# Kernel tuning notes

Measured on AMD Instinct MI355X. Metric: run time of the kernel, lower is better.

The kernel has to match this reference:

```python
import jax, jax.numpy as jnp
import numpy as np
from jax import lax

B = 512
THRESHOLD = 0.5
CFG = [64, 64, 'M', 128, 128, 'M', 256, 256, 256, 'M', 512, 512, 512, 'M', 512, 512, 512, 'M']  # VGG16


def _conv_relu(x, w, b):
    # x: [B,C,H,W], w: [O,I,3,3] (torch OIHW layout), pad=1 stride=1
    y = lax.conv_general_dilated(x, w, (1, 1), 'SAME',
                                 dimension_numbers=('NCHW', 'OIHW', 'NCHW'))
    return jax.nn.relu(y + b[None, :, None, None])


def _maxpool2(x):
    return lax.reduce_window(x, -jnp.inf, lax.max, (1, 1, 2, 2), (1, 1, 2, 2), 'VALID')


def _features(x, ws, bs):
    i = 0
    for c in CFG:
        if c == 'M':
            x = _maxpool2(x)
        else:
            x = _conv_relu(x, ws[i], bs[i])
            i += 1
    return x  # [B,512,1,1]


def _gcn(distance):
    # Faithful translation, including the source bug: 'onetensor' is zeros_like,
    # so mask==0 everywhere and A_hat collapses to the identity.
    n = distance.shape[0]
    zero = jnp.zeros_like(distance)
    one = jnp.zeros_like(distance)  # bug in original: torch.zeros_like for onetensor
    adj = jnp.where(distance > THRESHOLD, distance, zero)
    mask = jnp.where(distance > THRESHOLD, one, zero)
    idx = lax.top_k(adj, 10)[1]                                   # [n,10]
    top10 = jnp.zeros_like(adj).at[jnp.arange(n)[:, None], idx].set(1.0)
    top10 = top10 * mask
    a_hat = top10 + jnp.eye(n, dtype=distance.dtype)
    d_inv = jnp.diag(1.0 / jnp.sum(a_hat, axis=1))
    return lax.stop_gradient(a_hat @ d_inv)                        # [n,n]


def _forward(x, target, conv_ws, conv_bs, lin1_w, lin1_b, lin2_w, lin2_b, cls_w, cls_b):
    feat = _features(x, conv_ws, conv_bs).reshape(x.shape[0], -1)  # [B,512]
    h = jax.nn.relu(feat @ lin1_w + lin1_b)                        # [B,256]
    low = h @ lin2_w + lin2_b                                      # [B,128]
    graph_pre = jax.nn.sigmoid(low @ low.T)                        # [B,B]
    graph_gt = (target[:, None] == target[None, :]).astype(jnp.float32)
    mat = _gcn(graph_pre)                                          # [B,B], detached
    out = (mat @ feat) @ cls_w + cls_b                             # [B,10]
    return out, graph_pre, graph_gt


def setup_inputs() -> dict:
    key = jax.random.key(0)
    ks = iter(jax.random.split(key, 64))
    inp = {}
    inp['x'] = jax.random.normal(next(ks), (B, 3, 32, 32), dtype=jnp.float32)
    inp['target'] = jax.random.randint(next(ks), (B,), 0, 10)
    in_c, i = 3, 0
    for c in CFG:
        if c == 'M':
            continue
        scale = 1.0 / np.sqrt(in_c * 9.0)
        inp['conv%d_w' % i] = jax.random.normal(next(ks), (c, in_c, 3, 3), dtype=jnp.float32) * scale
        inp['conv%d_b' % i] = jnp.zeros((c,), dtype=jnp.float32)
        in_c, i = c, i + 1
    inp['lin1_w'] = jax.random.normal(next(ks), (512, 256), dtype=jnp.float32) * (1.0 / np.sqrt(512.0))
    inp['lin1_b'] = jnp.zeros((256,), dtype=jnp.float32)
    inp['lin2_w'] = jax.random.normal(next(ks), (256, 128), dtype=jnp.float32) * (1.0 / np.sqrt(256.0))
    inp['lin2_b'] = jnp.zeros((128,), dtype=jnp.float32)
    inp['cls_w'] = jax.random.normal(next(ks), (512, 10), dtype=jnp.float32) * (1.0 / np.sqrt(512.0))
    inp['cls_b'] = jnp.zeros((10,), dtype=jnp.float32)
    return inp


def reference(x, target,
              conv0_w, conv0_b, conv1_w, conv1_b, conv2_w, conv2_b, conv3_w, conv3_b,
              conv4_w, conv4_b, conv5_w, conv5_b, conv6_w, conv6_b, conv7_w, conv7_b,
              conv8_w, conv8_b, conv9_w, conv9_b, conv10_w, conv10_b, conv11_w, conv11_b,
              conv12_w, conv12_b,
              lin1_w, lin1_b, lin2_w, lin2_b, cls_w, cls_b):
    ws = [conv0_w, conv1_w, conv2_w, conv3_w, conv4_w, conv5_w, conv6_w,
          conv7_w, conv8_w, conv9_w, conv10_w, conv11_w, conv12_w]
    bs = [conv0_b, conv1_b, conv2_b, conv3_b, conv4_b, conv5_b, conv6_b,
          conv7_b, conv8_b, conv9_b, conv10_b, conv11_b, conv12_b]
    return _forward(x, target, ws, bs, lin1_w, lin1_b, lin2_w, lin2_b, cls_w, cls_b)
```

## Files before the change

### kernel.cpp

```cpp
#include <hip/hip_runtime.h>

typedef unsigned short u16;
typedef __bf16 bf16x8 __attribute__((ext_vector_type(8)));
typedef float floatx4 __attribute__((ext_vector_type(4)));

__device__ inline u16 f2bf(float f) {
    return __builtin_bit_cast(u16, (__bf16)f);
}
__device__ inline float bf2f(u16 h) {
    return __uint_as_float(((unsigned int)h) << 16);
}

__device__ __forceinline__ void async_copy16(u16* lds, const u16* g) {
    __builtin_amdgcn_global_load_lds(
        (const __attribute__((address_space(1))) unsigned int*)(uintptr_t)g,
        (__attribute__((address_space(3))) unsigned int*)(unsigned int)(uintptr_t)lds,
        16, 0, 0);
}

__global__ void zero_halo(u16* __restrict__ buf, int Hp, int C, int total8)
{
    int i = blockIdx.x * 256 + threadIdx.x;
    if (i >= total8) return;
    int c8 = i % (C / 8);
    int p  = i / (C / 8);
    int ring = 4 * Hp - 4;
    int h = p % ring;
    int b = p / ring;
    int y, x;
    if (h < Hp)              { y = 0;              x = h; }
    else if (h < 2 * Hp)     { y = Hp - 1;         x = h - Hp; }
    else if (h < 3 * Hp - 2) { y = h - 2 * Hp + 1; x = 0; }
    else                     { y = h - 3 * Hp + 3; x = Hp - 1; }
    uint4 z = make_uint4(0u, 0u, 0u, 0u);
    *(uint4*)(buf + ((size_t)((b * Hp + y) * Hp + x) * C) + c8 * 8) = z;
}

__global__ __launch_bounds__(256) void conv0_kernel(
    const float* __restrict__ x, const float* __restrict__ w,
    const float* __restrict__ bias, u16* __restrict__ out)
{
    __shared__ __align__(16) float xs[3][6][36];
    const int t  = threadIdx.x;
    const int b  = blockIdx.x >> 3;
    const int y0 = (blockIdx.x & 7) * 4;

    for (int i = t; i < 3 * 6 * 36; i += 256) {
        int ci  = i / 216;
        int rem = i % 216;
        int r   = rem / 36;
        int c   = rem % 36;
        int gy  = y0 - 1 + r;
        int gx  = c - 1;
        float v = 0.f;
        if ((unsigned)gy < 32u && (unsigned)gx < 32u)
            v = x[((b * 3 + ci) * 32 + gy) * 32 + gx];
        xs[ci][r][c] = v;
    }
    const int lane = t & 63;
    const int wv   = t >> 6;
    float wr[27];
    #pragma unroll
    for (int k = 0; k < 27; k++) wr[k] = w[lane * 27 + k];
    const float bz = bias[lane];
    __syncthreads();

    const int y = y0 + wv;
    u16* orow = out + ((size_t)((b * 34 + y + 1) * 34 + 1) * 64) + lane;
    for (int xg = 0; xg < 32; xg += 4) {
        float a0 = bz, a1 = bz, a2 = bz, a3 = bz;
        #pragma unroll
        for (int ci = 0; ci < 3; ci++) {
            #pragma unroll
            for (int rr = 0; rr < 3; rr++) {
                const float* row = &xs[ci][wv + rr][0];
                float4 c03 = *(const float4*)(row + xg);
                float2 c45 = *(const float2*)(row + xg + 4);
                float w0 = wr[ci * 9 + rr * 3 + 0];
                float w1 = wr[ci * 9 + rr * 3 + 1];
                float w2 = wr[ci * 9 + rr * 3 + 2];
                a0 += c03.x * w0 + c03.y * w1 + c03.z * w2;
                a1 += c03.y * w0 + c03.z * w1 + c03.w * w2;
                a2 += c03.z * w0 + c03.w * w1 + c45.x * w2;
                a3 += c03.w * w0 + c45.x * w1 + c45.y * w2;
            }
        }
        orow[(xg + 0) * 64] = f2bf(fmaxf(a0, 0.f));
        orow[(xg + 1) * 64] = f2bf(fmaxf(a1, 0.f));
        orow[(xg + 2) * 64] = f2bf(fmaxf(a2, 0.f));
        orow[(xg + 3) * 64] = f2bf(fmaxf(a3, 0.f));
    }
}

struct RepackArgs {
    const float* src[14];
    u16* dst[14];
    int p1[14];
    int p2[14];
    int startBlk[15];
    int nseg;
};

__global__ __launch_bounds__(256) void repack_all(RepackArgs a)
{
    __shared__ __align__(16) u16 lds[9216];
    int blk = blockIdx.x;
    int s = 0;
    #pragma unroll 1
    while (s + 1 < a.nseg && blk >= a.startBlk[s + 1]) s++;
    const int cb = blk - a.startBlk[s];
    const int t  = threadIdx.x;

    if (a.p2[s] == 0) {
        const int Cin = a.p1[s];
        const int logCin = __builtin_ctz(Cin);
        const float* src = a.src[s] + (size_t)cb * 9216;
        u16* dst = a.dst[s] + (size_t)cb * 9216;
        #pragma unroll
        for (int it = 0; it < 9; it++) {
            int j4 = it * 256 + t;
            float4 v = *(const float4*)(src + j4 * 4);
            ushort4 h;
            h.x = f2bf(v.x); h.y = f2bf(v.y); h.z = f2bf(v.z); h.w = f2bf(v.w);
            *(ushort4*)(lds + j4 * 4) = h;
        }
        __syncthreads();
        #pragma unroll
        for (int it = 0; it < 9; it++) {
            int o4   = (it * 256 + t) * 4;
            int ci   = o4 & (Cin - 1);
            int rest = o4 >> logCin;
            int co   = rest / 9;
            int sh   = rest - co * 9;
            int sb   = (co << logCin) * 9 + ci * 9 + sh;
            ushort4 h;
            h.x = lds[sb]; h.y = lds[sb + 9]; h.z = lds[sb + 18]; h.w = lds[sb + 27];
            *(ushort4*)(dst + o4) = h;
        }
    } else {
        const int K = a.p1[s], N = a.p2[s];
        const int ntx = N >> 6;
        const int k0 = (cb / ntx) * 64, n0 = (cb % ntx) * 64;
        const float* src = a.src[s];
        u16* dst = a.dst[s];
        const int r = t >> 4, c4 = (t & 15) * 4;
        #pragma unroll
        for (int rr = 0; rr < 64; rr += 16) {
            float4 v = *(const float4*)(src + (size_t)(k0 + r + rr) * N + n0 + c4);
            u16* p = lds + (r + rr) * 72 + c4;
            p[0] = f2bf(v.x); p[1] = f2bf(v.y); p[2] = f2bf(v.z); p[3] = f2bf(v.w);
        }
        __syncthreads();
        #pragma unroll
        for (int it = 0; it < 2; it++) {
            int ov = it * 256 + t;
            int n  = ov >> 3;
            int kq = (ov & 7) * 8;
            __align__(16) u16 h[8];
            #pragma unroll
            for (int j = 0; j < 8; j++) h[j] = lds[(kq + j) * 72 + n];
            *(uint4*)(dst + (size_t)(n0 + n) * K + k0 + kq) = *(uint4*)h;
        }
    }
}

template <int BM, int BN>
__global__ __launch_bounds__(256) void conv_gemm(
    const u16* __restrict__ in, const u16* __restrict__ wt,
    const float* __restrict__ bias, u16* __restrict__ out,
    float* __restrict__ partial, size_t pstride,
    int H, int Cin, int Cout, int logHW, int logW, int splitN,
    int outPad, int poolMode)
{
    constexpr int BK = 64;
    constexpr int WC = (BM == 256) ? BN : (BN / 2);
    constexpr int NT = WC / 16;
    constexpr int NB_A = BM / 32;
    constexpr int NB_B = BN / 32;
    constexpr int ASZ = BM * BK;
    constexpr int BSZ = BN * BK;
    __shared__ u16 As[2 * ASZ];
    __shared__ u16 Bs[2 * BSZ];

    const int Nblocks = Cout / BN;
    const int per = gridDim.x >> 3;
    const int bid = (blockIdx.x & 7) * per + (blockIdx.x >> 3);
    const int sp   = bid % splitN;
    const int tile = bid / splitN;
    const int m0 = (tile / Nblocks) * BM;
    const int n0 = (tile % Nblocks) * BN;

    const int t    = threadIdx.x;
    const int lane = t & 63;
    const int wave = t >> 6;
    const int quad = lane >> 4;
    const int l16  = lane & 15;
    const int wm   = (BM == 256) ? wave : (wave >> 1);
    const int wn   = (BM == 256) ? 0 : (wave & 1);
    const int W    = H;
    const int Wp   = H + 2;
    const int HW   = 1 << logHW;
    const int col8 = t & 7;
    const int r0   = t >> 3;
    const int scol = col8 ^ (r0 & 7);

    const int CinB = Cin * 2;

    int vA[NB_A];
    #pragma unroll
    for (int j = 0; j < NB_A; j++) {
        int m  = m0 + r0 + 32 * j;
        int b  = m >> logHW;
        int rm = m & (HW - 1);
        int y  = rm >> logW;
        int xx = rm & (W - 1);
        vA[j] = ((b * Wp + y + 1) * Wp + xx + 1) * CinB + scol * 16;
    }
    int vB[NB_B];
    #pragma unroll
    for (int j = 0; j < NB_B; j++)
        vB[j] = (n0 + r0 + 32 * j) * 9 * CinB + scol * 16;

    const int logKB = (Cin == 64) ? 0 : (Cin == 128) ? 1 : (Cin == 256) ? 2 : 3;
    const int KB  = 1 << logKB;
    const int T   = 9 * KB;
    const int len = T / splitN;
    const int it0 = sp * len;

    int s0 = it0 >> logKB;
    int c3 = s0 - (s0 / 3) * 3;
    int ta = ((s0 / 3 - 1) * Wp + (c3 - 1)) * CinB;
    int kb = (it0 & (KB - 1)) * 128;
    int tb = it0 * 128;

    const char* const inB = (const char*)in;
    const char* const wtB = (const char*)wt;

    floatx4 acc[4][NT];
    #pragma unroll
    for (int i = 0; i < 4; i++)
        #pragma unroll
        for (int j = 0; j < NT; j++)
            acc[i][j] = (floatx4){0.f, 0.f, 0.f, 0.f};

    const int sw = (l16 & 7) * 8;

    auto stage = [&](int ua, int tbv, int buf) {
        u16* la = As + buf * ASZ + t * 8;
        u16* lb = Bs + buf * BSZ + t * 8;
        #pragma unroll
        for (int j = 0; j < NB_A; j++)
            async_copy16(la + j * 2048, (const u16*)(inB + (ua + vA[j])));
        #pragma unroll
        for (int j = 0; j < NB_B; j++)
            async_copy16(lb + j * 2048, (const u16*)(wtB + (tbv + vB[j])));
    };
    auto advance = [&]() {
        tb += 128;
        kb += 128;
        if (kb == CinB) {
            kb = 0;
            ta += (c3 == 2) ? (Wp - 2) * CinB : CinB;
            c3 = (c3 == 2) ? 0 : c3 + 1;
        }
    };

    stage(ta + kb, tb, 0);
    advance();
    __syncthreads();

    int cur = 0;
    for (int it = 0; it < len; it++) {
        if (it + 1 < len) {
            stage(ta + kb, tb, cur ^ 1);
            advance();
        }
        const u16* Ab = As + cur * ASZ;
        const u16* Bb = Bs + cur * BSZ;
        #pragma unroll
        for (int kk = 0; kk < BK; kk += 32) {
            bf16x8 af[4], bfv[NT];
            int cbo = kk + quad * 8;
            #pragma unroll
            for (int mt = 0; mt < 4; mt++)
                af[mt] = *(const bf16x8*)(Ab + (wm * 64 + mt * 16 + l16) * 64 + (cbo ^ sw));
            #pragma unroll
            for (int nt = 0; nt < NT; nt++)
                bfv[nt] = *(const bf16x8*)(Bb + (wn * WC + nt * 16 + l16) * 64 + (cbo ^ sw));
            #pragma unroll
            for (int mt = 0; mt < 4; mt++)
                #pragma unroll
                for (int nt = 0; nt < NT; nt++)
                    acc[mt][nt] = __builtin_amdgcn_mfma_f32_16x16x32_bf16(
                        af[mt], bfv[nt], acc[mt][nt], 0, 0, 0);
        }
        __syncthreads();
        cur ^= 1;
    }

    const int ngb = n0 + wn * WC + l16;

    if (splitN > 1) {
        float* pout = partial + (size_t)sp * pstride;
        #pragma unroll
        for (int mt = 0; mt < 4; mt++)
            #pragma unroll
            for (int r = 0; r < 4; r++) {
                int mg = m0 + wm * 64 + mt * 16 + quad * 4 + r;
                float* op = pout + (size_t)mg * Cout + ngb;
                #pragma unroll
                for (int nt = 0; nt < NT; nt++)
                    op[nt * 16] = acc[mt][nt][r];
            }
        return;
    }

    float bzv[NT];
    #pragma unroll
    for (int nt = 0; nt < NT; nt++) bzv[nt] = bias[ngb + nt * 16];

    if (poolMode) {
        const int Hpo = (H >> 1) + 2;
        if (logW == 5) {
            #pragma unroll
            for (int mt = 0; mt < 2; mt++)
                #pragma unroll
                for (int rp = 0; rp < 2; rp++) {
                    int m1 = m0 + wm * 64 + mt * 16 + quad * 4 + 2 * rp;
                    int b  = m1 >> logHW;
                    int rm = m1 & (HW - 1);
                    int yp = (rm >> logW) >> 1;
                    int xp = (rm & (W - 1)) >> 1;
                    u16* op = out + (size_t)((b * Hpo + yp + 1) * Hpo + xp + 1) * Cout + ngb;
                    #pragma unroll
                    for (int nt = 0; nt < NT; nt++) {
                        float v = fmaxf(
                            fmaxf(acc[mt][nt][2 * rp], acc[mt][nt][2 * rp + 1]),
                            fmaxf(acc[mt + 2][nt][2 * rp], acc[mt + 2][nt][2 * rp + 1]));
                        op[nt * 16] = f2bf(fmaxf(v + bzv[nt], 0.f));
                    }
                }
        } else if (logW == 4) {
            #pragma unroll
            for (int mtp = 0; mtp < 2; mtp++)
                #pragma unroll
                for (int rp = 0; rp < 2; rp++) {
                    int mt = 2 * mtp;
                    int m1 = m0 + wm * 64 + mt * 16 + quad * 4 + 2 * rp;
                    int b  = m1 >> logHW;
                    int rm = m1 & (HW - 1);
                    int yp = (rm >> logW) >> 1;
                    int xp = (rm & (W - 1)) >> 1;
                    u16* op = out + (size_t)((b * Hpo + yp + 1) * Hpo + xp + 1) * Cout + ngb;
                    #pragma unroll
                    for (int nt = 0; nt < NT; nt++) {
                        float v = fmaxf(
                            fmaxf(acc[mt][nt][2 * rp], acc[mt][nt][2 * rp + 1]),
                            fmaxf(acc[mt + 1][nt][2 * rp], acc[mt + 1][nt][2 * rp + 1]));
                        op[nt * 16] = f2bf(fmaxf(v + bzv[nt], 0.f));
                    }
                }
        } else {
            #pragma unroll
            for (int mt = 0; mt < 4; mt++)
                #pragma unroll
                for (int rp = 0; rp < 2; rp++) {
                    int m1 = m0 + wm * 64 + mt * 16 + quad * 4 + 2 * rp;
                    int b  = m1 >> logHW;
                    int rm = m1 & (HW - 1);
                    int yp = (rm >> logW) >> 1;
                    int xp = (rm & (W - 1)) >> 1;
                    u16* op = out + (size_t)((b * Hpo + yp + 1) * Hpo + xp + 1) * Cout + ngb;
                    #pragma unroll
                    for (int nt = 0; nt < NT; nt++) {
                        float a = fmaxf(acc[mt][nt][2 * rp], acc[mt][nt][2 * rp + 1]);
                        float p = __shfl_xor(a, 32, 64);
                        float v = fmaxf(a, p);
                        if (quad < 2)
                            op[nt * 16] = f2bf(fmaxf(v + bzv[nt], 0.f));
                    }
                }
        }
        return;
    }

    #pragma unroll
    for (int mt = 0; mt < 4; mt++) {
        #pragma unroll
        for (int r = 0; r < 4; r++) {
            int mg = m0 + wm * 64 + mt * 16 + quad * 4 + r;
            size_t obase;
            if (outPad) {
                int b  = mg >> logHW;
                int rm = mg & (HW - 1);
                int y  = rm >> logW;
                int xx = rm & (W - 1);
                obase = (size_t)((b * Wp + y + 1) * Wp + xx + 1) * Cout;
            } else {
                obase = (size_t)mg * Cout;
            }
            u16* op = out + obase + ngb;
            #pragma unroll
            for (int nt = 0; nt < NT; nt++)
                op[nt * 16] = f2bf(fmaxf(acc[mt][nt][r] + bzv[nt], 0.f));
        }
    }
}

template <int BM, int BN, int W, int CIN>
__global__ __launch_bounds__(256) void conv_halo(
    const u16* __restrict__ in, const u16* __restrict__ wt,
    const float* __restrict__ bias, u16* __restrict__ out,
    int outPad, int poolMode)
{
    constexpr int BK = 64;
    constexpr int WC = (BM == 256) ? BN : (BN / 2);
    constexpr int NT = WC / 16;
    constexpr int NB_B = BN / 32;
    constexpr int BSZ = BN * BK;
    constexpr int Wp = W + 2;
    constexpr int R  = BM / W;
    constexpr int P  = (R + 2) * Wp;
    constexpr int CinB = CIN * 2;
    constexpr int CH = CinB / 16;
    constexpr int LOG_CH = (CH == 8) ? 3 : 4;
    constexpr int HALO_CHUNKS = P * CH;
    constexpr int ROUNDS = (HALO_CHUNKS + 255) / 256;
    constexpr int logW = (W == 32) ? 5 : 4;
    constexpr int logHW = 2 * logW;
    constexpr int HW = 1 << logHW;
    constexpr int KB = CIN / 64;
    constexpr int T  = 9 * KB;

    __shared__ __align__(16) u16 Ah[P * CH * 8];
    __shared__ __align__(16) u16 Bs[2 * BSZ];

    constexpr int Nblocks = 1;
    static_assert(true, "");
    const int per = gridDim.x >> 3;
    const int bid = (blockIdx.x & 7) * per + (blockIdx.x >> 3);
    const int m0 = (bid / Nblocks) * BM;
    const int n0 = (bid % Nblocks) * BN;

    const int t    = threadIdx.x;
    const int lane = t & 63;
    const int wave = t >> 6;
    const int quad = lane >> 4;
    const int l16  = lane & 15;
    const int wm   = (BM == 256) ? wave : (wave >> 1);
    const int wn   = (BM == 256) ? 0 : (wave & 1);
    const int col8 = t & 7;
    const int r0   = t >> 3;
    const int scol = col8 ^ (r0 & 7);

    const int b  = m0 >> logHW;
    const int y0 = (m0 & (HW - 1)) >> logW;

    const char* hsrc = (const char*)in + (size_t)((b * Wp + y0) * Wp) * CinB;
    #pragma unroll
    for (int rd = 0; rd < ROUNDS; rd++) {
        int i = rd * 256 + t;
        if ((HALO_CHUNKS % 256 == 0) || i < HALO_CHUNKS) {
            int pp   = i >> LOG_CH;
            int si   = i ^ (pp & 7);
            async_copy16(Ah + i * 8, (const u16*)(hsrc + (size_t)si * 16));
        }
    }

    int vB[NB_B];
    #pragma unroll
    for (int j = 0; j < NB_B; j++)
        vB[j] = (n0 + r0 + 32 * j) * 9 * CinB + scol * 16;
    const char* const wtB = (const char*)wt;
    auto stageB = [&](int tbv, int buf) {
        u16* lb = Bs + buf * BSZ + t * 8;
        #pragma unroll
        for (int j = 0; j < NB_B; j++)
            async_copy16(lb + j * 2048, (const u16*)(wtB + (tbv + vB[j])));
    };

    int pBase[4];
    #pragma unroll
    for (int mt = 0; mt < 4; mt++) {
        int dm = wm * 64 + mt * 16 + l16;
        pBase[mt] = (dm >> logW) * Wp + (dm & (W - 1));
    }

    floatx4 acc[4][NT];
    #pragma unroll
    for (int i = 0; i < 4; i++)
        #pragma unroll
        for (int j = 0; j < NT; j++)
            acc[i][j] = (floatx4){0.f, 0.f, 0.f, 0.f};

    const int sw = (l16 & 7) * 8;
    const char* const AhB = (const char*)Ah;

    stageB(0, 0);
    __syncthreads();

    int cur = 0, tb = 128;
    int pOff = 0, c3 = 0, cb = 0;
    for (int it = 0; it < T; it++) {
        if (it + 1 < T) { stageB(tb, cur ^ 1); tb += 128; }
        const int pO = pOff, cbv = cb;
        cb += 128;
        if (cb == CinB) {
            cb = 0;
            pOff += (c3 == 2) ? (Wp - 2) : 1;
            c3 = (c3 == 2) ? 0 : c3 + 1;
        }

        bf16x8 af[2][4];
        #pragma unroll
        for (int mt = 0; mt < 4; mt++) {
            int p  = pBase[mt] + pO;
            int pc = p & 7;
            int ab = p * CinB + cbv;
            #pragma unroll
            for (int kk2 = 0; kk2 < 2; kk2++) {
                int kq = kk2 * 4 + quad;
                af[kk2][mt] = *(const bf16x8*)(AhB + ab + ((kq ^ pc) << 4));
            }
        }

        const u16* Bb = Bs + cur * BSZ;
        #pragma unroll
        for (int kk2 = 0; kk2 < 2; kk2++) {
            int cbo = kk2 * 32 + quad * 8;
            bf16x8 bfv[NT];
            #pragma unroll
            for (int nt = 0; nt < NT; nt++)
                bfv[nt] = *(const bf16x8*)(Bb + (wn * WC + nt * 16 + l16) * 64 + (cbo ^ sw));
            #pragma unroll
            for (int mt = 0; mt < 4; mt++)
                #pragma unroll
                for (int nt = 0; nt < NT; nt++)
                    acc[mt][nt] = __builtin_amdgcn_mfma_f32_16x16x32_bf16(
                        af[kk2][mt], bfv[nt], acc[mt][nt], 0, 0, 0);
        }
        __syncthreads();
        cur ^= 1;
    }

    const int ngb = n0 + wn * WC + l16;
    float bzv[NT];
    #pragma unroll
    for (int nt = 0; nt < NT; nt++) bzv[nt] = bias[ngb + nt * 16];
    const int Cout = BN;
    const int H = W;

    if (poolMode) {
        const int Hpo = (H >> 1) + 2;
        if (logW == 5) {
            #pragma unroll
            for (int mt = 0; mt < 2; mt++)
                #pragma unroll
                for (int rp = 0; rp < 2; rp++) {
                    int m1 = m0 + wm * 64 + mt * 16 + quad * 4 + 2 * rp;
                    int bb = m1 >> logHW;
                    int rm = m1 & (HW - 1);
                    int yp = (rm >> logW) >> 1;
                    int xp = (rm & (W - 1)) >> 1;
                    u16* op = out + (size_t)((bb * Hpo + yp + 1) * Hpo + xp + 1) * Cout + ngb;
                    #pragma unroll
                    for (int nt = 0; nt < NT; nt++) {
                        float v = fmaxf(
                            fmaxf(acc[mt][nt][2 * rp], acc[mt][nt][2 * rp + 1]),
                            fmaxf(acc[mt + 2][nt][2 * rp], acc[mt + 2][nt][2 * rp + 1]));
                        op[nt * 16] = f2bf(fmaxf(v + bzv[nt], 0.f));
                    }
                }
        } else {
            #pragma unroll
            for (int mtp = 0; mtp < 2; mtp++)
                #pragma unroll
                for (int rp = 0; rp < 2; rp++) {
                    int mt = 2 * mtp;
                    int m1 = m0 + wm * 64 + mt * 16 + quad * 4 + 2 * rp;
                    int bb = m1 >> logHW;
                    int rm = m1 & (HW - 1);
                    int yp = (rm >> logW) >> 1;
                    int xp = (rm & (W - 1)) >> 1;
                    u16* op = out + (size_t)((bb * Hpo + yp + 1) * Hpo + xp + 1) * Cout + ngb;
                    #pragma unroll
                    for (int nt = 0; nt < NT; nt++) {
                        float v = fmaxf(
                            fmaxf(acc[mt][nt][2 * rp], acc[mt][nt][2 * rp + 1]),
                            fmaxf(acc[mt + 1][nt][2 * rp], acc[mt + 1][nt][2 * rp + 1]));
                        op[nt * 16] = f2bf(fmaxf(v + bzv[nt], 0.f));
                    }
                }
        }
        return;
    }

    #pragma unroll
    for (int mt = 0; mt < 4; mt++) {
        #pragma unroll
        for (int r = 0; r < 4; r++) {
            int mg = m0 + wm * 64 + mt * 16 + quad * 4 + r;
            size_t obase;
            if (outPad) {
                int bb = mg >> logHW;
                int rm = mg & (HW - 1);
                int y  = rm >> logW;
                int xx = rm & (W - 1);
                obase = (size_t)((bb * Wp + y + 1) * Wp + xx + 1) * Cout;
            } else {
                obase = (size_t)mg * Cout;
            }
            u16* op = out + obase + ngb;
            #pragma unroll
            for (int nt = 0; nt < NT; nt++)
                op[nt * 16] = f2bf(fmaxf(acc[mt][nt][r] + bzv[nt], 0.f));
        }
    }
}

__global__ void reduce_split(const float* __restrict__ partial,
                             const float* __restrict__ bias, u16* __restrict__ out,
                             int MN, int C, int logC, int splitN, size_t pstride,
                             int H, int logHW, int logW, int outPad)
{
    int i4 = (blockIdx.x * 256 + threadIdx.x) * 4;
    if (i4 >= MN) return;
    float4 s = *(const float4*)(partial + i4);
    for (int sp = 1; sp < splitN; sp++) {
        float4 p = *(const float4*)(partial + (size_t)sp * pstride + i4);
        s.x += p.x; s.y += p.y; s.z += p.z; s.w += p.w;
    }
    int n = i4 & (C - 1);
    int m = i4 >> logC;
    size_t obase;
    if (outPad) {
        int Wp = H + 2;
        int b  = m >> logHW;
        int rm = m & ((1 << logHW) - 1);
        int y  = rm >> logW;
        int xx = rm & (H - 1);
        obase = (size_t)((b * Wp + y + 1) * Wp + xx + 1) * C;
    } else {
        obase = (size_t)m * C;
    }
    ushort4 o;
    o.x = f2bf(fmaxf(s.x + bias[n + 0], 0.f));
    o.y = f2bf(fmaxf(s.y + bias[n + 1], 0.f));
    o.z = f2bf(fmaxf(s.z + bias[n + 2], 0.f));
    o.w = f2bf(fmaxf(s.w + bias[n + 3], 0.f));
    *(ushort4*)(out + obase + n) = o;
}

__global__ void reduce_pool(const float* __restrict__ partial,
                            const float* __restrict__ bias, u16* __restrict__ out,
                            int total4, int C, int splitN, size_t pstride,
                            int H, int outPad)
{
    int idx = blockIdx.x * 256 + threadIdx.x;
    if (idx >= total4) return;
    int c4 = idx % (C / 4);
    int p  = idx / (C / 4);
    int Ho = H >> 1;
    int xp = p % Ho; p /= Ho;
    int yp = p % Ho;
    int b  = p / Ho;
    int n  = c4 * 4;
    float4 best;
    bool first = true;
    #pragma unroll
    for (int dy = 0; dy < 2; dy++)
        #pragma unroll
        for (int dx = 0; dx < 2; dx++) {
            int m = (b * H + 2 * yp + dy) * H + 2 * xp + dx;
            const float* q = partial + (size_t)m * C + n;
            float4 s = *(const float4*)q;
            for (int sp = 1; sp < splitN; sp++) {
                float4 pp = *(const float4*)(q + (size_t)sp * pstride);
                s.x += pp.x; s.y += pp.y; s.z += pp.z; s.w += pp.w;
            }
            if (first) { best = s; first = false; }
            else {
                best.x = fmaxf(best.x, s.x); best.y = fmaxf(best.y, s.y);
                best.z = fmaxf(best.z, s.z); best.w = fmaxf(best.w, s.w);
            }
        }
    size_t obase;
    if (outPad) {
        int Hpo = Ho + 2;
        obase = (size_t)((b * Hpo + yp + 1) * Hpo + xp + 1) * C;
    } else {
        obase = (size_t)((b * Ho + yp) * Ho + xp) * C;
    }
    ushort4 o;
    o.x = f2bf(fmaxf(best.x + bias[n + 0], 0.f));
    o.y = f2bf(fmaxf(best.y + bias[n + 1], 0.f));
    o.z = f2bf(fmaxf(best.z + bias[n + 2], 0.f));
    o.w = f2bf(fmaxf(best.w + bias[n + 3], 0.f));
    *(ushort4*)(out + obase + n) = o;
}

template <bool RELU, bool OUTBF>
__global__ __launch_bounds__(256) void gemm64(
    const u16* __restrict__ A, const u16* __restrict__ Bt,
    const float* __restrict__ bias, void* __restrict__ outv,
    int M, int N, int K)
{
    constexpr int LDP = 72;
    __shared__ u16 As[64 * LDP];
    __shared__ u16 Bs[64 * LDP];

    const int nb = N >> 6;
    const int m0 = (blockIdx.x / nb) * 64;
    const int n0 = (blockIdx.x % nb) * 64;
    const int t = threadIdx.x, lane = t & 63, wave = t >> 6;
    const int quad = lane >> 4, l16 = lane & 15;
    const int wm = wave >> 1, wn = wave & 1;
    const int col8 = t & 7, r0 = t >> 3;

    floatx4 acc[2][2];
    #pragma unroll
    for (int i = 0; i < 2; i++)
        #pragma unroll
        for (int j = 0; j < 2; j++)
            acc[i][j] = (floatx4){0.f, 0.f, 0.f, 0.f};

    for (int kb = 0; kb < K; kb += 64) {
        #pragma unroll
        for (int j = 0; j < 2; j++) {
            int row = r0 + 32 * j;
            *(uint4*)(As + row * LDP + col8 * 8) =
                *(const uint4*)(A + (size_t)(m0 + row) * K + kb + col8 * 8);
            *(uint4*)(Bs + row * LDP + col8 * 8) =
                *(const uint4*)(Bt + (size_t)(n0 + row) * K + kb + col8 * 8);
        }
        __syncthreads();
        #pragma unroll
        for (int kk = 0; kk < 64; kk += 32) {
            bf16x8 af[2], bfv[2];
            #pragma unroll
            for (int mt = 0; mt < 2; mt++)
                af[mt] = *(const bf16x8*)(As + (wm * 32 + mt * 16 + l16) * LDP + kk + quad * 8);
            #pragma unroll
            for (int nt = 0; nt < 2; nt++)
                bfv[nt] = *(const bf16x8*)(Bs + (wn * 32 + nt * 16 + l16) * LDP + kk + quad * 8);
            #pragma unroll
            for (int mt = 0; mt < 2; mt++)
                #pragma unroll
                for (int nt = 0; nt < 2; nt++)
                    acc[mt][nt] = __builtin_amdgcn_mfma_f32_16x16x32_bf16(
                        af[mt], bfv[nt], acc[mt][nt], 0, 0, 0);
        }
        __syncthreads();
    }
    #pragma unroll
    for (int mt = 0; mt < 2; mt++) {
        #pragma unroll
        for (int nt = 0; nt < 2; nt++) {
            #pragma unroll
            for (int r = 0; r < 4; r++) {
                int mg = m0 + wm * 32 + mt * 16 + quad * 4 + r;
                int ng = n0 + wn * 32 + nt * 16 + l16;
                float v = acc[mt][nt][r] + bias[ng];
                if (RELU) v = fmaxf(v, 0.f);
                if (OUTBF) ((u16*)outv)[(size_t)mg * N + ng] = f2bf(v);
                else       ((float*)outv)[(size_t)mg * N + ng] = v;
            }
        }
    }
}

__global__ __launch_bounds__(256) void graph_tile(
    const float* __restrict__ low, const int* __restrict__ target,
    float* __restrict__ gpre, float* __restrict__ ggt)
{
    __shared__ float Al[64 * 132];
    __shared__ float Bl[128 * 68];
    const int t = threadIdx.x;
    const int gr0 = (blockIdx.x >> 3) * 64;
    const int gc0 = (blockIdx.x & 7) * 64;

    #pragma unroll
    for (int j = 0; j < 32; j++) {
        int flat = t + 256 * j;
        int k = flat & 127;
        int rc = flat >> 7;
        Al[rc * 132 + k] = low[(size_t)(gr0 + rc) * 128 + k];
        Bl[k * 68 + rc]  = low[(size_t)(gc0 + rc) * 128 + k];
    }
    __syncthreads();

    const int tx = t & 15, ty = t >> 4;
    float acc[4][4];
    #pragma unroll
    for (int r = 0; r < 4; r++)
        #pragma unroll
        for (int c = 0; c < 4; c++) acc[r][c] = 0.f;

    for (int k = 0; k < 128; k++) {
        float a[4], b[4];
        #pragma unroll
        for (int r = 0; r < 4; r++) a[r] = Al[(ty * 4 + r) * 132 + k];
        #pragma unroll
        for (int c = 0; c < 4; c++) b[c] = Bl[k * 68 + tx * 4 + c];
        #pragma unroll
        for (int r = 0; r < 4; r++)
            #pragma unroll
            for (int c = 0; c < 4; c++) acc[r][c] += a[r] * b[c];
    }
    #pragma unroll
    for (int r = 0; r < 4; r++) {
        int row = gr0 + ty * 4 + r;
        int tr  = target[row];
        float4 gp, gg;
        float* pp = (float*)&gp;
        float* gg_ = (float*)&gg;
        #pragma unroll
        for (int c = 0; c < 4; c++) {
            pp[c]  = 1.f / (1.f + __expf(-acc[r][c]));
            gg_[c] = (tr == target[gc0 + tx * 4 + c]) ? 1.f : 0.f;
        }
        *(float4*)(gpre + (size_t)row * 512 + gc0 + tx * 4) = gp;
        *(float4*)(ggt  + (size_t)row * 512 + gc0 + tx * 4) = gg;
    }
}

__global__ __launch_bounds__(256) void cls_kernel(
    const u16* __restrict__ feat, const float* __restrict__ w,
    const float* __restrict__ bias, float* __restrict__ out)
{
    __shared__ float ws[5120];
    const int t = threadIdx.x;
    for (int i = t; i < 5120; i += 256) ws[i] = w[i];
    __syncthreads();
    const int lane = t & 63;
    const int row  = blockIdx.x * 4 + (t >> 6);
    float a[10];
    #pragma unroll
    for (int j = 0; j < 10; j++) a[j] = 0.f;
    #pragma unroll
    for (int i = 0; i < 8; i++) {
        int k = i * 64 + lane;
        float f = bf2f(feat[(size_t)row * 512 + k]);
        #pragma unroll
        for (int j = 0; j < 10; j++) a[j] += f * ws[k * 10 + j];
    }
    #pragma unroll
    for (int j = 0; j < 10; j++)
        #pragma unroll
        for (int off = 32; off > 0; off >>= 1)
            a[j] += __shfl_down(a[j], off, 64);
    if (lane == 0) {
        #pragma unroll
        for (int j = 0; j < 10; j++) out[row * 10 + j] = a[j] + bias[j];
    }
}

extern "C" void kernel_launch(void* const* d_in, const int* in_sizes, int n_in,
                              void* d_out, int out_size, void* d_ws, size_t ws_size,
                              hipStream_t stream)
{
    const float* x      = (const float*)d_in[0];
    const int*   target = (const int*)d_in[1];
    const float* conv_w[13];
    const float* conv_b[13];
    for (int i = 0; i < 13; i++) {
        conv_w[i] = (const float*)d_in[2 + 2 * i];
        conv_b[i] = (const float*)d_in[3 + 2 * i];
    }
    const float* lin1_w = (const float*)d_in[28];
    const float* lin1_b = (const float*)d_in[29];
    const float* lin2_w = (const float*)d_in[30];
    const float* lin2_b = (const float*)d_in[31];
    const float* cls_w  = (const float*)d_in[32];
    const float* cls_b  = (const float*)d_in[33];
    float* out = (float*)d_out;

    static const int cin_arr[13]  = {3, 64, 64, 128, 128, 256, 256, 256, 512, 512, 512, 512, 512};
    static const int cout_arr[13] = {64, 64, 128, 128, 256, 256, 256, 512, 512, 512, 512, 512, 512};

    char* ws = (char*)d_ws;
    size_t off = 0;
    const size_t R0SZ = (size_t)512 * 34 * 34 * 64 * 2;
    const size_t R1SZ = (size_t)512 * 34 * 34 * 64 * 2;
    char* R0raw = ws + off; off += R0SZ;
    char* R1raw = ws + off; off += R1SZ;
    u16* R0 = (u16*)R0raw;
    u16* R1 = (u16*)R1raw;
    float* PA = (float*)(R0raw + 20971520);
    float* PB = (float*)(R1raw + 20971520);
    u16* wt[13];
    for (int i = 1; i < 13; i++) {
        wt[i] = (u16*)(ws + off);
        off += (size_t)cout_arr[i] * 9 * cin_arr[i] * 2;
    }
    u16* wtl1 = (u16*)(ws + off); off += (size_t)256 * 512 * 2;
    u16* wtl2 = (u16*)(ws + off); off += (size_t)128 * 256 * 2;
    u16* hbuf = (u16*)(ws + off); off += (size_t)512 * 256 * 2;
    float* lowbuf = (float*)(ws + off); off += (size_t)512 * 128 * 4;

    RepackArgs ra;
    int nb = 0, blk = 0;
    ra.startBlk[0] = 0;
    for (int i = 1; i < 13; i++) {
        ra.src[nb] = conv_w[i];
        ra.dst[nb] = wt[i];
        ra.p1[nb] = cin_arr[i];
        ra.p2[nb] = 0;
        blk += cout_arr[i] * cin_arr[i] / 1024;
        nb++; ra.startBlk[nb] = blk;
    }
    ra.src[nb] = lin1_w; ra.dst[nb] = wtl1; ra.p1[nb] = 512; ra.p2[nb] = 256;
    blk += (512 / 64) * (256 / 64);
    nb++; ra.startBlk[nb] = blk;
    ra.src[nb] = lin2_w; ra.dst[nb] = wtl2; ra.p1[nb] = 256; ra.p2[nb] = 128;
    blk += (256 / 64) * (128 / 64);
    nb++; ra.startBlk[nb] = blk;
    ra.nseg = nb;
    repack_all<<<blk, 256, 0, stream>>>(ra);

    auto zh = [&](u16* buf, int Hp, int C) {
        int total8 = 512 * (4 * Hp - 4) * (C / 8);
        zero_halo<<<(total8 + 255) / 256, 256, 0, stream>>>(buf, Hp, C, total8);
    };
    auto launch_conv = [&](int li, int Hl, int bm, int bn, u16* inb, u16* outb,
                           float* part, int splitN, int outPad, int poolMode) {
        int Cin = cin_arr[li], Cout = cout_arr[li];
        int M = 512 * Hl * Hl;
        int logW = __builtin_ctz(Hl);
        int logHW = 2 * logW;
        size_t pstride = (size_t)M * Cout;
        int grid = (M / bm) * (Cout / bn) * splitN;
        if (bm == 256) {
            conv_gemm<256, 64><<<grid, 256, 0, stream>>>(
                inb, wt[li], conv_b[li], outb, part, pstride,
                Hl, Cin, Cout, logHW, logW, splitN, outPad, poolMode);
        } else if (bn == 128) {
            conv_gemm<128, 128><<<grid, 256, 0, stream>>>(
                inb, wt[li], conv_b[li], outb, part, pstride,
                Hl, Cin, Cout, logHW, logW, splitN, outPad, poolMode);
        } else {
            conv_gemm<128, 64><<<grid, 256, 0, stream>>>(
                inb, wt[li], conv_b[li], outb, part, pstride,
                Hl, Cin, Cout, logHW, logW, splitN, outPad, poolMode);
        }
    };
    auto launch_reduce = [&](int li, int Hl, u16* outb, float* part, int splitN, int outPad) {
        int Cout = cout_arr[li];
        int M = 512 * Hl * Hl;
        int logW = __builtin_ctz(Hl);
        size_t pstride = (size_t)M * Cout;
        int MN = M * Cout;
        reduce_split<<<(MN / 4 + 255) / 256, 256, 0, stream>>>(
            part, conv_b[li], outb, MN, Cout, __builtin_ctz(Cout),
            splitN, pstride, Hl, 2 * logW, logW, outPad);
    };
    auto launch_reduce_pool = [&](int li, int Hl, u16* outb, float* part, int splitN, int outPad) {
        int Cout = cout_arr[li];
        int M = 512 * Hl * Hl;
        size_t pstride = (size_t)M * Cout;
        int total4 = 512 * (Hl / 2) * (Hl / 2) * Cout / 4;
        reduce_pool<<<(total4 + 255) / 256, 256, 0, stream>>>(
            part, conv_b[li], outb, total4, Cout, splitN, pstride, Hl, outPad);
    };

    zh(R0, 34, 64);
    conv0_kernel<<<512 * 8, 256, 0, stream>>>(x, conv_w[0], conv_b[0], R0);

    zh(R1, 18, 64);
    conv_halo<256, 64, 32, 64><<<2048, 256, 0, stream>>>(
        R0, wt[1], conv_b[1], R1, 0, 1);
    zh(R0, 18, 128);
    conv_halo<128, 128, 16, 64><<<1024, 256, 0, stream>>>(
        R1, wt[2], conv_b[2], R0, 1, 0);
    zh(R1, 10, 128);
    conv_halo<128, 128, 16, 128><<<1024, 256, 0, stream>>>(
        R0, wt[3], conv_b[3], R1, 0, 1);
    zh(R0, 10, 256);
    launch_conv(4, 8, 128, 128, R1, R0, nullptr, 1, 1, 0);
    zh(R1, 10, 256);
    launch_conv(5, 8, 128, 128, R0, R1, nullptr, 1, 1, 0);
    zh(R0, 6, 256);
    launch_conv(6, 8, 128, 128, R1, R0, nullptr, 1, 0, 1);
    zh(R1, 6, 512);
    launch_conv(7, 4, 128, 128, R0, R1, PB, 2, 1, 0);
    launch_reduce(7, 4, R1, PB, 2, 1);
    zh(R0, 6, 512);
    launch_conv(8, 4, 128, 128, R1, R0, PA, 2, 1, 0);
    launch_reduce(8, 4, R0, PA, 2, 1);
    zh(R1, 4, 512);
    launch_conv(9, 4, 128, 128, R0, R1, PB, 2, 0, 0);
    launch_reduce_pool(9, 4, R1, PB, 2, 1);
    zh(R0, 4, 512);
    launch_conv(10, 2, 128, 64, R1, R0, PA, 4, 1, 0);
    launch_reduce(10, 2, R0, PA, 4, 1);
    zh(R1, 4, 512);
    launch_conv(11, 2, 128, 64, R0, R1, PB, 4, 1, 0);
    launch_reduce(11, 2, R1, PB, 4, 1);
    launch_conv(12, 2, 128, 64, R1, R0, PA, 4, 0, 0);
    launch_reduce_pool(12, 2, R0, PA, 4, 0);

    u16* feat = R0;
    gemm64<true, true><<<(512 / 64) * (256 / 64), 256, 0, stream>>>(
        feat, wtl1, lin1_b, hbuf, 512, 256, 512);
    gemm64<false, false><<<(512 / 64) * (128 / 64), 256, 0, stream>>>(
        hbuf, wtl2, lin2_b, lowbuf, 512, 128, 256);
    graph_tile<<<64, 256, 0, stream>>>(lowbuf, target, out + 5120, out + 5120 + 262144);
    cls_kernel<<<128, 256, 0, stream>>>(feat, cls_w, cls_b, out);
}
```

Measured before the change: 683.1 us.

## Rewrite first conv layer as bf16 MFMA im2col GEMM

Replaces the scalar FP32 direct convolution for the 3-channel first layer with an im2col formulation. Each block stages 8 input rows in LDS, builds 16x32 bf16 A fragments through an offset table, and runs 16x16x32 bf16 MFMAs against the 64 output channels with K=27 zero-padded to 32. The goal is to move the conv0 FLOPs from VALU FMAs onto matrix cores. In exchange, inputs and weights are rounded to bf16 before accumulation instead of computed in FP32, and the output stores are scattered 2-byte writes.

New measurement: 672.8 us. No clear change (-1.5%).

```diff
diff --git a/kernel.cpp b/kernel.cpp
--- a/kernel.cpp
+++ b/kernel.cpp
@@ -36,18 +36,19 @@
     *(uint4*)(buf + ((size_t)((b * Hp + y) * Hp + x) * C) + c8 * 8) = z;
 }
 
-__global__ __launch_bounds__(256) void conv0_kernel(
+__global__ __launch_bounds__(256) void conv0_mfma(
     const float* __restrict__ x, const float* __restrict__ w,
     const float* __restrict__ bias, u16* __restrict__ out)
 {
-    __shared__ __align__(16) float xs[3][6][36];
+    __shared__ __align__(16) float xsf[3 * 10 * 36];
+    __shared__ int tab[32];
     const int t  = threadIdx.x;
-    const int b  = blockIdx.x >> 3;
-    const int y0 = (blockIdx.x & 7) * 4;
-
-    for (int i = t; i < 3 * 6 * 36; i += 256) {
-        int ci  = i / 216;
-        int rem = i % 216;
+    const int b  = blockIdx.x >> 2;
+    const int y0 = (blockIdx.x & 3) * 8;
+
+    for (int i = t; i < 3 * 10 * 36; i += 256) {
+        int ci  = i / 360;
+        int rem = i % 360;
         int r   = rem / 36;
         int c   = rem % 36;
         int gy  = y0 - 1 + r;
@@ -55,40 +56,94 @@
         float v = 0.f;
         if ((unsigned)gy < 32u && (unsigned)gx < 32u)
             v = x[((b * 3 + ci) * 32 + gy) * 32 + gx];
-        xs[ci][r][c] = v;
-    }
+        xsf[i] = v;
+    }
+    if (t < 32) {
+        int k = t, off = 0;
+        if (k < 27) {
+            int ci = k / 9;
+            int r9 = k - ci * 9;
+            int rr = r9 / 3;
+            int cc = r9 - rr * 3;
+            off = (ci * 10 + rr) * 36 + cc;
+        }
+        tab[t] = off;
+    }
+
     const int lane = t & 63;
     const int wv   = t >> 6;
-    float wr[27];
-    #pragma unroll
-    for (int k = 0; k < 27; k++) wr[k] = w[lane * 27 + k];
-    const float bz = bias[lane];
+    const int quad = lane >> 4;
+    const int l16  = lane & 15;
+    const int q8   = quad * 8;
+
+    bf16x8 bf[4];
+    #pragma unroll
+    for (int nt = 0; nt < 4; nt++) {
+        int col = nt * 16 + l16;
+        u16 hh[8];
+        #pragma unroll
+        for (int j = 0; j < 8; j++) {
+            int k = q8 + j;
+            float wv_ = (k < 27) ? w[col * 27 + k] : 0.f;
+            hh[j] = f2bf(wv_);
+        }
+        #pragma unroll
+        for (int j = 0; j < 8; j++) ((u16*)&bf[nt])[j] = hh[j];
+    }
+    float bzv[4];
+    #pragma unroll
+    for (int nt = 0; nt < 4; nt++) bzv[nt] = bias[nt * 16 + l16];
+
     __syncthreads();
 
-    const int y = y0 + wv;
-    u16* orow = out + ((size_t)((b * 34 + y + 1) * 34 + 1) * 64) + lane;
-    for (int xg = 0; xg < 32; xg += 4) {
-        float a0 = bz, a1 = bz, a2 = bz, a3 = bz;
-        #pragma unroll
-        for (int ci = 0; ci < 3; ci++) {
-            #pragma unroll
-            for (int rr = 0; rr < 3; rr++) {
-                const float* row = &xs[ci][wv + rr][0];
-                float4 c03 = *(const float4*)(row + xg);
-                float2 c45 = *(const float2*)(row + xg + 4);
-                float w0 = wr[ci * 9 + rr * 3 + 0];
-                float w1 = wr[ci * 9 + rr * 3 + 1];
-                float w2 = wr[ci * 9 + rr * 3 + 2];
-                a0 += c03.x * w0 + c03.y * w1 + c03.z * w2;
-                a1 += c03.y * w0 + c03.z * w1 + c03.w * w2;
-                a2 += c03.z * w0 + c03.w * w1 + c45.x * w2;
-                a3 += c03.w * w0 + c45.x * w1 + c45.y * w2;
-            }
-        }
-        orow[(xg + 0) * 64] = f2bf(fmaxf(a0, 0.f));
-        orow[(xg + 1) * 64] = f2bf(fmaxf(a1, 0.f));
-        orow[(xg + 2) * 64] = f2bf(fmaxf(a2, 0.f));
-        orow[(xg + 3) * 64] = f2bf(fmaxf(a3, 0.f));
+    int tb_[8];
+    #pragma unroll
+    for (int j = 0; j < 8; j++) tb_[j] = tab[q8 + j];
+
+    bf16x8 af[4];
+    #pragma unroll
+    for (int mt = 0; mt < 4; mt++) {
+        int dm   = wv * 64 + mt * 16 + l16;
+        int yloc = dm >> 5;
+        int xx   = dm & 31;
+        int bix  = yloc * 36 + xx;
+        u16 hh[8];
+        #pragma unroll
+        for (int j = 0; j < 8; j++) hh[j] = f2bf(xsf[bix + tb_[j]]);
+        if (quad == 3) {
+            #pragma unroll
+            for (int j = 3; j < 8; j++) hh[j] = 0;
+        }
+        #pragma unroll
+        for (int j = 0; j < 8; j++) ((u16*)&af[mt])[j] = hh[j];
+    }
+
+    floatx4 acc[4][4];
+    #pragma unroll
+    for (int i = 0; i < 4; i++)
+        #pragma unroll
+        for (int j = 0; j < 4; j++)
+            acc[i][j] = (floatx4){0.f, 0.f, 0.f, 0.f};
+
+    #pragma unroll
+    for (int mt = 0; mt < 4; mt++)
+        #pragma unroll
+        for (int nt = 0; nt < 4; nt++)
+            acc[mt][nt] = __builtin_amdgcn_mfma_f32_16x16x32_bf16(
+                af[mt], bf[nt], acc[mt][nt], 0, 0, 0);
+
+    #pragma unroll
+    for (int mt = 0; mt < 4; mt++) {
+        #pragma unroll
+        for (int r = 0; r < 4; r++) {
+            int p  = wv * 64 + mt * 16 + quad * 4 + r;
+            int y  = y0 + (p >> 5);
+            int xx = p & 31;
+            u16* op = out + (size_t)((b * 34 + y + 1) * 34 + xx + 1) * 64 + l16;
+            #pragma unroll
+            for (int nt = 0; nt < 4; nt++)
+                op[nt * 16] = f2bf(fmaxf(acc[mt][nt][r] + bzv[nt], 0.f));
+        }
     }
 }
 
@@ -964,7 +1019,7 @@
     };
 
     zh(R0, 34, 64);
-    conv0_kernel<<<512 * 8, 256, 0, stream>>>(x, conv_w[0], conv_b[0], R0);
+    conv0_mfma<<<512 * 4, 256, 0, stream>>>(x, conv_w[0], conv_b[0], R0);
 
     zh(R1, 18, 64);
     conv_halo<256, 64, 32, 64><<<2048, 256, 0, stream>>>(
```
